# Performance work log

Hardware: AMD Instinct MI355X
Metric: run time of the kernel (lower is better)

The kernel has to match this reference:

```python
import jax, jax.numpy as jnp
import numpy as np

B = 32
NODES = [200000, 1024, 256, 32]
CH = [1, 32, 64, 128]
EDGES = [2048000, 262144, 8192]
NCLS = 10


def _wn(V, g):
    # PyTorch weight_norm (dim=0): each output row rescaled to norm g[o]
    return g[:, None] * V / jnp.linalg.norm(V, axis=1, keepdims=True)


def _fgl(x, src, dst, n_out, W, b):
    # x: (B, C_in, N_in); sparse random-adjacency downsample then channel mix
    xt = jnp.moveaxis(x, 2, 0)                                   # (N_in, B, C_in)
    gathered = xt[src]                                           # (E, B, C_in)
    pooled = jax.ops.segment_sum(gathered, dst, num_segments=n_out)  # (N_out, B, C_in)
    return jnp.einsum('nbc,oc->bon', pooled, W) + b[None, :, None]   # (B, C_out, N_out)


def setup_inputs() -> dict:
    key = jax.random.key(0)
    ks = jax.random.split(key, 20)
    d = {}
    d['x'] = jax.random.normal(ks[0], (B, NODES[0]), jnp.float32)
    for i in range(3):
        e = EDGES[i]
        n_in, n_out = NODES[i], NODES[i + 1]
        d[f'edge_src{i}'] = jax.random.randint(ks[1 + 2 * i], (e,), 0, n_in, jnp.int32)
        d[f'edge_dst{i}'] = jnp.sort(jax.random.randint(ks[2 + 2 * i], (e,), 0, n_out, jnp.int32))
    for i in range(3):
        cin, cout = CH[i], CH[i + 1]
        d[f'V{i}'] = jax.random.normal(ks[7 + 3 * i], (cout, cin), jnp.float32) * 0.1
        d[f'g{i}'] = jnp.ones((cout,), jnp.float32)
        d[f'b{i}'] = jnp.zeros((cout,), jnp.float32)
    d['Vfc'] = jax.random.normal(ks[16], (NCLS, CH[-1] * NODES[-1]), jnp.float32) * 0.02
    d['gfc'] = jnp.ones((NCLS,), jnp.float32)
    d['bfc'] = jnp.zeros((NCLS,), jnp.float32)
    return d


def reference(x, edge_src0, edge_dst0, edge_src1, edge_dst1, edge_src2, edge_dst2,
              V0, g0, b0, V1, g1, b1, V2, g2, b2, Vfc, gfc, bfc):
    z = x[:, None, :]                                            # (B, 1, N_in)
    z = _fgl(z, edge_src0, edge_dst0, NODES[1], _wn(V0, g0), b0)  # (B, 32, 1024)
    z = _fgl(z, edge_src1, edge_dst1, NODES[2], _wn(V1, g1), b1)  # (B, 64, 256)
    z = _fgl(z, edge_src2, edge_dst2, NODES[3], _wn(V2, g2), b2)  # (B, 128, 32)
    flat = z.reshape(z.shape[0], -1)                             # (B, 4096)
    return flat @ _wn(Vfc, gfc).T + bfc                          # (B, NCLS)
```

## Files before the change

### kernel.cpp

```cpp
#include <hip/hip_runtime.h>
#include <math.h>

#define N0 200000
#define N1 1024
#define N2 256
#define N3 32
#define NE0 2048000
#define NE1 262144
#define NE2 8192
#define BATCH 32
#define NCLS 10
#define NB 4
#define SRC_PER_B 50000

typedef _Float16 h2 __attribute__((ext_vector_type(2)));
typedef _Float16 h8 __attribute__((ext_vector_type(8)));

__device__ __forceinline__ int lower_bound_i(const int* __restrict__ a, int n, int key) {
    int lo = 0, hi = n;
    while (lo < hi) {
        int mid = (lo + hi) >> 1;
        if (a[mid] < key) lo = mid + 1; else hi = mid;
    }
    return lo;
}

__global__ __launch_bounds__(256) void k_transpose(const float* __restrict__ x,
                                                   h2* __restrict__ xt) {
    __shared__ float tile[32][65];
    const int col0 = blockIdx.x * 64;
    const int tid = threadIdx.x;
    const int c = tid & 63, r0 = tid >> 6;
    #pragma unroll
    for (int r = r0; r < 32; r += 4) {
        int col = col0 + c;
        tile[r][c] = (col < N0) ? x[r * N0 + col] : 0.f;
    }
    __syncthreads();
    const int bb = (tid & 15) * 2, c0 = tid >> 4;
    #pragma unroll
    for (int cc = c0; cc < 64; cc += 16) {
        int col = col0 + cc;
        if (col < N0) {
            h2 v;
            v[0] = (_Float16)tile[bb][cc];
            v[1] = (_Float16)tile[bb + 1][cc];
            xt[col * 16 + (bb >> 1)] = v;
        }
    }
}

__global__ __launch_bounds__(256) void k_partition(const int* __restrict__ src,
                                                   const int* __restrict__ dst,
                                                   int* __restrict__ esrc,
                                                   int* __restrict__ bstart) {
    const int n = blockIdx.x;
    const int tid = threadIdx.x;
    const int e0 = lower_bound_i(dst, NE0, n);
    const int e1 = lower_bound_i(dst, NE0, n + 1);
    const int len = e1 - e0;
    const int wave = tid >> 6, lane = tid & 63;
    const int q0 = e0 + (len * wave) / 4;
    const int q1 = e0 + (len * (wave + 1)) / 4;
    __shared__ int wcnt[4][NB];
    __shared__ int wbase[4][NB];

    int c0 = 0, c1 = 0, c2 = 0, c3 = 0;
    for (int base = q0; base < q1; base += 64) {
        int e = base + lane;
        int b = -1;
        if (e < q1) b = src[e] / SRC_PER_B;
        c0 += __popcll(__ballot(b == 0));
        c1 += __popcll(__ballot(b == 1));
        c2 += __popcll(__ballot(b == 2));
        c3 += __popcll(__ballot(b == 3));
    }
    if (lane == 0) { wcnt[wave][0] = c0; wcnt[wave][1] = c1; wcnt[wave][2] = c2; wcnt[wave][3] = c3; }
    __syncthreads();
    if (tid == 0) {
        int acc = e0;
        #pragma unroll
        for (int b = 0; b < NB; ++b) {
            bstart[n * (NB + 1) + b] = acc;
            #pragma unroll
            for (int w = 0; w < 4; ++w) { wbase[w][b] = acc; acc += wcnt[w][b]; }
        }
        bstart[n * (NB + 1) + NB] = acc;
    }
    __syncthreads();

    int u0 = wbase[wave][0], u1 = wbase[wave][1], u2 = wbase[wave][2], u3 = wbase[wave][3];
    for (int base = q0; base < q1; base += 64) {
        int e = base + lane;
        int s = 0, b = -1;
        if (e < q1) { s = src[e]; b = s / SRC_PER_B; }
        unsigned long long m0 = __ballot(b == 0);
        unsigned long long m1 = __ballot(b == 1);
        unsigned long long m2 = __ballot(b == 2);
        unsigned long long m3 = __ballot(b == 3);
        unsigned long long lt = (1ull << lane) - 1ull;
        if (b == 0)      esrc[u0 + __popcll(m0 & lt)] = s;
        else if (b == 1) esrc[u1 + __popcll(m1 & lt)] = s;
        else if (b == 2) esrc[u2 + __popcll(m2 & lt)] = s;
        else if (b == 3) esrc[u3 + __popcll(m3 & lt)] = s;
        u0 += __popcll(m0); u1 += __popcll(m1); u2 += __popcll(m2); u3 += __popcll(m3);
    }
}

__global__ __launch_bounds__(128) void k_gather0s(const h8* __restrict__ table,
                                                  const int* __restrict__ esrc,
                                                  const int* __restrict__ bstart,
                                                  float* __restrict__ part) {
    const int b = blockIdx.x & (NB - 1);
    const int n = blockIdx.x >> 2;
    const int q0 = bstart[n * (NB + 1) + b];
    const int q1 = bstart[n * (NB + 1) + b + 1];
    const int tid = threadIdx.x;
    const int b4 = tid & 3;
    const int g  = tid >> 2;
    float acc[8] = {0.f, 0.f, 0.f, 0.f, 0.f, 0.f, 0.f, 0.f};
    int e = q0 + g;
    for (; e + 96 < q1; e += 128) {
        int s0 = __builtin_nontemporal_load(esrc + e);
        int s1 = __builtin_nontemporal_load(esrc + e + 32);
        int s2 = __builtin_nontemporal_load(esrc + e + 64);
        int s3 = __builtin_nontemporal_load(esrc + e + 96);
        h8 v0 = table[s0 * 4 + b4];
        h8 v1 = table[s1 * 4 + b4];
        h8 v2 = table[s2 * 4 + b4];
        h8 v3 = table[s3 * 4 + b4];
        #pragma unroll
        for (int i = 0; i < 8; ++i)
            acc[i] += (float)v0[i] + (float)v1[i] + (float)v2[i] + (float)v3[i];
    }
    for (; e < q1; e += 32) {
        int s = __builtin_nontemporal_load(esrc + e);
        h8 v = table[s * 4 + b4];
        #pragma unroll
        for (int i = 0; i < 8; ++i) acc[i] += (float)v[i];
    }
    __shared__ float red[32][33];
    #pragma unroll
    for (int i = 0; i < 8; ++i) red[g][b4 * 8 + i] = acc[i];
    __syncthreads();
    #pragma unroll
    for (int s = 16; s >= 1; s >>= 1) {
        if (g < s) {
            #pragma unroll
            for (int i = 0; i < 8; ++i)
                red[g][b4 * 8 + i] += red[g + s][b4 * 8 + i];
        }
        __syncthreads();
    }
    if (tid < 32) part[(b * N1 + n) * 32 + tid] = red[0][tid];
}

__global__ __launch_bounds__(256) void k_reduceP(const float* __restrict__ part,
                                                 _Float16* __restrict__ out) {
    int i = blockIdx.x * 256 + threadIdx.x;
    float s = part[i] + part[N1 * 32 + i] + part[2 * N1 * 32 + i] + part[3 * N1 * 32 + i];
    out[i] = (_Float16)s;
}

__global__ __launch_bounds__(256) void k_gather1(const h8* __restrict__ table,
                                                 const int* __restrict__ src,
                                                 const int* __restrict__ dst,
                                                 _Float16* __restrict__ out_h,
                                                 float* __restrict__ cnt_out) {
    const int n = blockIdx.x;
    const int e0 = lower_bound_i(dst, NE1, n);
    const int e1 = lower_bound_i(dst, NE1, n + 1);
    const int tid = threadIdx.x;
    const int b4 = tid & 3;
    const int g  = tid >> 2;
    float acc[8] = {0.f, 0.f, 0.f, 0.f, 0.f, 0.f, 0.f, 0.f};
    int e = e0 + g;
    for (; e + 192 < e1; e += 256) {
        int s0 = src[e];
        int s1 = src[e + 64];
        int s2 = src[e + 128];
        int s3 = src[e + 192];
        h8 v0 = table[s0 * 4 + b4];
        h8 v1 = table[s1 * 4 + b4];
        h8 v2 = table[s2 * 4 + b4];
        h8 v3 = table[s3 * 4 + b4];
        #pragma unroll
        for (int i = 0; i < 8; ++i)
            acc[i] += (float)v0[i] + (float)v1[i] + (float)v2[i] + (float)v3[i];
    }
    for (; e < e1; e += 64) {
        int s = src[e];
        h8 v = table[s * 4 + b4];
        #pragma unroll
        for (int i = 0; i < 8; ++i) acc[i] += (float)v[i];
    }
    __shared__ float red[64][33];
    #pragma unroll
    for (int i = 0; i < 8; ++i) red[g][b4 * 8 + i] = acc[i];
    __syncthreads();
    #pragma unroll
    for (int s = 32; s >= 1; s >>= 1) {
        if (g < s) {
            #pragma unroll
            for (int i = 0; i < 8; ++i)
                red[g][b4 * 8 + i] += red[g + s][b4 * 8 + i];
        }
        __syncthreads();
    }
    if (tid < 32) out_h[n * 32 + tid] = (_Float16)red[0][tid];
    else if (tid == 32) cnt_out[n] = (float)(e1 - e0);
}

__global__ __launch_bounds__(256) void k_gather2(const h8* __restrict__ table,
                                                 const int* __restrict__ src,
                                                 const int* __restrict__ dst,
                                                 const float* __restrict__ cnt_in,
                                                 float* __restrict__ out_f,
                                                 float* __restrict__ cnt_out,
                                                 float* __restrict__ t_out) {
    const int n = blockIdx.x;
    const int e0 = lower_bound_i(dst, NE2, n);
    const int e1 = lower_bound_i(dst, NE2, n + 1);
    const int tid = threadIdx.x;
    const int b4 = tid & 3;
    const int g  = tid >> 2;
    float acc[8] = {0.f, 0.f, 0.f, 0.f, 0.f, 0.f, 0.f, 0.f};
    float tacc = 0.f;
    for (int e = e0 + g; e < e1; e += 64) {
        int s = src[e];
        h8 v = table[s * 4 + b4];
        #pragma unroll
        for (int i = 0; i < 8; ++i) acc[i] += (float)v[i];
        if (b4 == 0) tacc += cnt_in[s];
    }
    __shared__ float red[64][33];
    __shared__ float tred[64];
    #pragma unroll
    for (int i = 0; i < 8; ++i) red[g][b4 * 8 + i] = acc[i];
    if (b4 == 0) tred[g] = tacc;
    __syncthreads();
    #pragma unroll
    for (int s = 32; s >= 1; s >>= 1) {
        if (g < s) {
            #pragma unroll
            for (int i = 0; i < 8; ++i)
                red[g][b4 * 8 + i] += red[g + s][b4 * 8 + i];
            if (b4 == 0) tred[g] += tred[g + s];
        }
        __syncthreads();
    }
    if (tid < 32) out_f[n * 32 + tid] = red[0][tid];
    else if (tid == 32) cnt_out[n] = (float)(e1 - e0);
    else if (tid == 33) t_out[n] = tred[0];
}

__global__ __launch_bounds__(256) void k_out(
    const float* __restrict__ V0, const float* __restrict__ g0, const float* __restrict__ b0,
    const float* __restrict__ V1, const float* __restrict__ g1, const float* __restrict__ b1,
    const float* __restrict__ V2, const float* __restrict__ g2, const float* __restrict__ b2,
    const float* __restrict__ Vfc, const float* __restrict__ gfc, const float* __restrict__ bfc,
    const float* __restrict__ S2, const float* __restrict__ T2, const float* __restrict__ cnt2,
    float* __restrict__ out) {
    const int k = blockIdx.x;
    const int tid = threadIdx.x;
    __shared__ float w0[32], u[64], v[64], p[128], q[128], r[128];
    __shared__ float redA[8][32], redB[8][32], redC[8][32], redD[8][32];
    __shared__ float nnred[4];
    __shared__ float M[32];
    __shared__ float scale_s, Kc_s;

    if (tid < 32) {
        float val = V0[tid];
        w0[tid] = g0[tid] * val / fabsf(val);
    }
    __syncthreads();
    if (tid < 64) {
        float nn = 0.f;
        #pragma unroll
        for (int c = 0; c < 32; ++c) { float t = V1[tid * 32 + c]; nn += t * t; }
        float inv = g1[tid] * rsqrtf(nn);
        float su = 0.f, sv = 0.f;
        #pragma unroll
        for (int c = 0; c < 32; ++c) {
            float w = V1[tid * 32 + c] * inv;
            su += w * w0[c]; sv += w * b0[c];
        }
        u[tid] = su; v[tid] = sv;
    }
    __syncthreads();
    if (tid < 128) {
        float nn = 0.f;
        #pragma unroll
        for (int c = 0; c < 64; ++c) { float t = V2[tid * 64 + c]; nn += t * t; }
        float inv = g2[tid] * rsqrtf(nn);
        float sp = 0.f, sq = 0.f, sr = 0.f;
        #pragma unroll
        for (int c = 0; c < 64; ++c) {
            float w = V2[tid * 64 + c] * inv;
            sp += w * u[c]; sq += w * v[c]; sr += w * b1[c];
        }
        p[tid] = sp; q[tid] = sq; r[tid] = sr;
    }
    __syncthreads();

    const int n3 = tid & 31, og = tid >> 5;
    float nn = 0.f, mk = 0.f, mq = 0.f, mr = 0.f, mb = 0.f;
    #pragma unroll
    for (int i = 0; i < 16; ++i) {
        int o = og + 8 * i;
        float w = Vfc[k * 4096 + tid + 256 * i];
        nn += w * w;
        mk += w * p[o]; mq += w * q[o]; mr += w * r[o]; mb += w * b2[o];
    }
    #pragma unroll
    for (int off = 32; off; off >>= 1) nn += __shfl_xor(nn, off);
    if ((tid & 63) == 0) nnred[tid >> 6] = nn;
    redA[og][n3] = mk; redB[og][n3] = mq; redC[og][n3] = mr; redD[og][n3] = mb;
    __syncthreads();
    if (tid == 0) {
        float s = nnred[0] + nnred[1] + nnred[2] + nnred[3];
        scale_s = gfc[k] * rsqrtf(s);
    }
    __syncthreads();
    if (tid < 32) {
        float smk = 0.f, smq = 0.f, smr = 0.f, smb = 0.f;
        #pragma unroll
        for (int i = 0; i < 8; ++i) {
            smk += redA[i][tid]; smq += redB[i][tid];
            smr += redC[i][tid]; smb += redD[i][tid];
        }
        float scale = scale_s;
        M[tid] = scale * smk;
        float kcp = scale * (smq * T2[tid] + smr * cnt2[tid] + smb);
        #pragma unroll
        for (int off = 16; off; off >>= 1) kcp += __shfl_xor(kcp, off);
        if (tid == 0) Kc_s = kcp + bfc[k];
    }
    __syncthreads();
    if (tid < 32) {
        int b = tid;
        float s = 0.f;
        #pragma unroll
        for (int n = 0; n < 32; ++n) s += M[n] * S2[n * 32 + b];
        out[b * NCLS + k] = s + Kc_s;
    }
}

extern "C" void kernel_launch(void* const* d_in, const int* in_sizes, int n_in,
                              void* d_out, int out_size, void* d_ws, size_t ws_size,
                              hipStream_t stream) {
    const float* x   = (const float*)d_in[0];
    const int* src0  = (const int*)d_in[1];
    const int* dst0  = (const int*)d_in[2];
    const int* src1  = (const int*)d_in[3];
    const int* dst1  = (const int*)d_in[4];
    const int* src2  = (const int*)d_in[5];
    const int* dst2  = (const int*)d_in[6];
    const float* V0  = (const float*)d_in[7];
    const float* g0  = (const float*)d_in[8];
    const float* b0  = (const float*)d_in[9];
    const float* V1  = (const float*)d_in[10];
    const float* g1  = (const float*)d_in[11];
    const float* b1  = (const float*)d_in[12];
    const float* V2  = (const float*)d_in[13];
    const float* g2  = (const float*)d_in[14];
    const float* b2  = (const float*)d_in[15];
    const float* Vfc = (const float*)d_in[16];
    const float* gfc = (const float*)d_in[17];
    const float* bfc = (const float*)d_in[18];

    char* ws = (char*)d_ws;
    _Float16* xt  = (_Float16*)(ws);
    int* esrc     = (int*)(ws + 12800000);
    int* bstart   = (int*)(ws + 20992000);
    float* P0p    = (float*)(ws + 21012480);
    _Float16* P0h = (_Float16*)(ws + 21536768);
    _Float16* S1h = (_Float16*)(ws + 21602304);
    float* cnt1   = (float*)(ws + 21618688);
    float* S2     = (float*)(ws + 21619712);
    float* T2     = (float*)(ws + 21623808);
    float* cnt2   = (float*)(ws + 21623936);

    k_transpose<<<(N0 + 63) / 64, 256, 0, stream>>>(x, (h2*)xt);
    k_partition<<<N1, 256, 0, stream>>>(src0, dst0, esrc, bstart);
    k_gather0s<<<N1 * NB, 128, 0, stream>>>((const h8*)xt, esrc, bstart, P0p);
    k_reduceP<<<(N1 * 32) / 256, 256, 0, stream>>>(P0p, P0h);
    k_gather1<<<N2, 256, 0, stream>>>((const h8*)P0h, src1, dst1, S1h, cnt1);
    k_gather2<<<N3, 256, 0, stream>>>((const h8*)S1h, src2, dst2, cnt1,
                                      S2, cnt2, T2);
    k_out<<<NCLS, 256, 0, stream>>>(V0, g0, b0, V1, g1, b1, V2, g2, b2,
                                    Vfc, gfc, bfc, S2, T2, cnt2, (float*)d_out);
}
```

Measured before the change: 81.41 us.

## Merge transpose with partition and fold partial reduction into gather1

Combines the transpose and edge-partition kernels into one launch that dispatches on block index, so the two independent pre-passes run concurrently. The four per-bucket partials from gather0 are now stored as fp16 and summed inside gather1 as it reads them, which removes the separate reduceP kernel. Gather0 also switches from nontemporal loads to plain loads of the edge sources. This saves two launches and a full pass over the partial buffer, at the cost of gather1 making four table reads per edge and rounding each partial to fp16 before summing.

```diff
diff --git a/kernel.cpp b/kernel.cpp
--- a/kernel.cpp
+++ b/kernel.cpp
@@ -12,6 +12,7 @@
 #define NCLS 10
 #define NB 4
 #define SRC_PER_B 50000
+#define TBLOCKS 3125
 
 typedef _Float16 h2 __attribute__((ext_vector_type(2)));
 typedef _Float16 h8 __attribute__((ext_vector_type(8)));
@@ -25,37 +26,37 @@
     return lo;
 }
 
-__global__ __launch_bounds__(256) void k_transpose(const float* __restrict__ x,
-                                                   h2* __restrict__ xt) {
-    __shared__ float tile[32][65];
-    const int col0 = blockIdx.x * 64;
-    const int tid = threadIdx.x;
-    const int c = tid & 63, r0 = tid >> 6;
-    #pragma unroll
-    for (int r = r0; r < 32; r += 4) {
-        int col = col0 + c;
-        tile[r][c] = (col < N0) ? x[r * N0 + col] : 0.f;
-    }
-    __syncthreads();
-    const int bb = (tid & 15) * 2, c0 = tid >> 4;
-    #pragma unroll
-    for (int cc = c0; cc < 64; cc += 16) {
-        int col = col0 + cc;
-        if (col < N0) {
-            h2 v;
-            v[0] = (_Float16)tile[bb][cc];
-            v[1] = (_Float16)tile[bb + 1][cc];
-            xt[col * 16 + (bb >> 1)] = v;
-        }
-    }
-}
-
-__global__ __launch_bounds__(256) void k_partition(const int* __restrict__ src,
-                                                   const int* __restrict__ dst,
-                                                   int* __restrict__ esrc,
-                                                   int* __restrict__ bstart) {
-    const int n = blockIdx.x;
-    const int tid = threadIdx.x;
+__global__ __launch_bounds__(256) void k_pre(const float* __restrict__ x,
+                                             h2* __restrict__ xt,
+                                             const int* __restrict__ src,
+                                             const int* __restrict__ dst,
+                                             int* __restrict__ esrc,
+                                             int* __restrict__ bstart) {
+    const int tid = threadIdx.x;
+    if (blockIdx.x < TBLOCKS) {
+        __shared__ float tile[32][65];
+        const int col0 = blockIdx.x * 64;
+        const int c = tid & 63, r0 = tid >> 6;
+        #pragma unroll
+        for (int r = r0; r < 32; r += 4) {
+            int col = col0 + c;
+            tile[r][c] = (col < N0) ? x[r * N0 + col] : 0.f;
+        }
+        __syncthreads();
+        const int bb = (tid & 15) * 2, c0 = tid >> 4;
+        #pragma unroll
+        for (int cc = c0; cc < 64; cc += 16) {
+            int col = col0 + cc;
+            if (col < N0) {
+                h2 v;
+                v[0] = (_Float16)tile[bb][cc];
+                v[1] = (_Float16)tile[bb + 1][cc];
+                xt[col * 16 + (bb >> 1)] = v;
+            }
+        }
+        return;
+    }
+    const int n = blockIdx.x - TBLOCKS;
     const int e0 = lower_bound_i(dst, NE0, n);
     const int e1 = lower_bound_i(dst, NE0, n + 1);
     const int len = e1 - e0;
@@ -110,7 +111,7 @@
 __global__ __launch_bounds__(128) void k_gather0s(const h8* __restrict__ table,
                                                   const int* __restrict__ esrc,
                                                   const int* __restrict__ bstart,
-                                                  float* __restrict__ part) {
+                                                  _Float16* __restrict__ p0p) {
     const int b = blockIdx.x & (NB - 1);
     const int n = blockIdx.x >> 2;
     const int q0 = bstart[n * (NB + 1) + b];
@@ -121,10 +122,10 @@
     float acc[8] = {0.f, 0.f, 0.f, 0.f, 0.f, 0.f, 0.f, 0.f};
     int e = q0 + g;
     for (; e + 96 < q1; e += 128) {
-        int s0 = __builtin_nontemporal_load(esrc + e);
-        int s1 = __builtin_nontemporal_load(esrc + e + 32);
-        int s2 = __builtin_nontemporal_load(esrc + e + 64);
-        int s3 = __builtin_nontemporal_load(esrc + e + 96);
+        int s0 = esrc[e];
+        int s1 = esrc[e + 32];
+        int s2 = esrc[e + 64];
+        int s3 = esrc[e + 96];
         h8 v0 = table[s0 * 4 + b4];
         h8 v1 = table[s1 * 4 + b4];
         h8 v2 = table[s2 * 4 + b4];
@@ -134,7 +135,7 @@
             acc[i] += (float)v0[i] + (float)v1[i] + (float)v2[i] + (float)v3[i];
     }
     for (; e < q1; e += 32) {
-        int s = __builtin_nontemporal_load(esrc + e);
+        int s = esrc[e];
         h8 v = table[s * 4 + b4];
         #pragma unroll
         for (int i = 0; i < 8; ++i) acc[i] += (float)v[i];
@@ -152,17 +153,10 @@
         }
         __syncthreads();
     }
-    if (tid < 32) part[(b * N1 + n) * 32 + tid] = red[0][tid];
-}
-
-__global__ __launch_bounds__(256) void k_reduceP(const float* __restrict__ part,
-                                                 _Float16* __restrict__ out) {
-    int i = blockIdx.x * 256 + threadIdx.x;
-    float s = part[i] + part[N1 * 32 + i] + part[2 * N1 * 32 + i] + part[3 * N1 * 32 + i];
-    out[i] = (_Float16)s;
-}
-
-__global__ __launch_bounds__(256) void k_gather1(const h8* __restrict__ table,
+    if (tid < 32) p0p[(b * N1 + n) * 32 + tid] = (_Float16)red[0][tid];
+}
+
+__global__ __launch_bounds__(256) void k_gather1(const h8* __restrict__ p0p,
                                                  const int* __restrict__ src,
                                                  const int* __restrict__ dst,
                                                  _Float16* __restrict__ out_h,
@@ -174,25 +168,15 @@
     const int b4 = tid & 3;
     const int g  = tid >> 2;
     float acc[8] = {0.f, 0.f, 0.f, 0.f, 0.f, 0.f, 0.f, 0.f};
-    int e = e0 + g;
-    for (; e + 192 < e1; e += 256) {
-        int s0 = src[e];
-        int s1 = src[e + 64];
-        int s2 = src[e + 128];
-        int s3 = src[e + 192];
-        h8 v0 = table[s0 * 4 + b4];
-        h8 v1 = table[s1 * 4 + b4];
-        h8 v2 = table[s2 * 4 + b4];
-        h8 v3 = table[s3 * 4 + b4];
+    for (int e = e0 + g; e < e1; e += 64) {
+        int s = src[e];
+        h8 v0 = p0p[0 * N1 * 4 + s * 4 + b4];
+        h8 v1 = p0p[1 * N1 * 4 + s * 4 + b4];
+        h8 v2 = p0p[2 * N1 * 4 + s * 4 + b4];
+        h8 v3 = p0p[3 * N1 * 4 + s * 4 + b4];
         #pragma unroll
         for (int i = 0; i < 8; ++i)
-            acc[i] += (float)v0[i] + (float)v1[i] + (float)v2[i] + (float)v3[i];
-    }
-    for (; e < e1; e += 64) {
-        int s = src[e];
-        h8 v = table[s * 4 + b4];
-        #pragma unroll
-        for (int i = 0; i < 8; ++i) acc[i] += (float)v[i];
+            acc[i] += ((float)v0[i] + (float)v1[i]) + ((float)v2[i] + (float)v3[i]);
     }
     __shared__ float red[64][33];
     #pragma unroll
@@ -370,22 +354,20 @@
     const float* bfc = (const float*)d_in[18];
 
     char* ws = (char*)d_ws;
-    _Float16* xt  = (_Float16*)(ws);
-    int* esrc     = (int*)(ws + 12800000);
-    int* bstart   = (int*)(ws + 20992000);
-    float* P0p    = (float*)(ws + 21012480);
-    _Float16* P0h = (_Float16*)(ws + 21536768);
-    _Float16* S1h = (_Float16*)(ws + 21602304);
-    float* cnt1   = (float*)(ws + 21618688);
-    float* S2     = (float*)(ws + 21619712);
-    float* T2     = (float*)(ws + 21623808);
-    float* cnt2   = (float*)(ws + 21623936);
-
-    k_transpose<<<(N0 + 63) / 64, 256, 0, stream>>>(x, (h2*)xt);
-    k_partition<<<N1, 256, 0, stream>>>(src0, dst0, esrc, bstart);
-    k_gather0s<<<N1 * NB, 128, 0, stream>>>((const h8*)xt, esrc, bstart, P0p);
-    k_reduceP<<<(N1 * 32) / 256, 256, 0, stream>>>(P0p, P0h);
-    k_gather1<<<N2, 256, 0, stream>>>((const h8*)P0h, src1, dst1, S1h, cnt1);
+    _Float16* xt   = (_Float16*)(ws);
+    int* esrc      = (int*)(ws + 12800000);
+    int* bstart    = (int*)(ws + 20992000);
+    _Float16* P0p  = (_Float16*)(ws + 21012480);
+    _Float16* S1h  = (_Float16*)(ws + 21274624);
+    float* cnt1    = (float*)(ws + 21291008);
+    float* S2      = (float*)(ws + 21292032);
+    float* T2      = (float*)(ws + 21296128);
+    float* cnt2    = (float*)(ws + 21296256);
+
+    k_pre<<<TBLOCKS + N1, 256, 0, stream>>>(x, (h2*)xt, src0, dst0, esrc, bstart);
+    k_gather0s<<<N1 * NB, 128, 0, stream>>>((const h8*)xt, esrc, bstart,
+                                            (_Float16*)P0p);
+    k_gather1<<<N2, 256, 0, stream>>>((const h8*)P0p, src1, dst1, S1h, cnt1);
     k_gather2<<<N3, 256, 0, stream>>>((const h8*)S1h, src2, dst2, cnt1,
                                       S2, cnt2, T2);
     k_out<<<NCLS, 256, 0, stream>>>(V0, g0, b0, V1, g1, b1, V2, g2, b2,
```

Result: faster. 79.11 us (-2.8%).
